# Performance work log

Measured on AMD Instinct MI355X. Metric: run time of the kernel, lower is better.

The kernel has to match this reference:

```python
import jax, jax.numpy as jnp
import numpy as np

B, N, K, F = 1, 50000, 16, 128
EPS = 1e-5

def _bn(h, gamma, beta):
    # BatchNorm1d in training mode: per-feature-channel stats over (batch, nodes)
    mean = jnp.mean(h, axis=(0, 1), keepdims=True)
    var = jnp.var(h, axis=(0, 1), keepdims=True)
    return (h - mean) * jax.lax.rsqrt(var + EPS) * gamma + beta

def _rgcn(h, neighbors, W, b):
    # pad one zero node row, gather K neighbors per node, flatten, linear
    h_pad = jnp.pad(h, ((0, 0), (0, 1), (0, 0)))           # [B, N+1, F]
    gathered = h_pad[:, neighbors]                          # [B, N, K, F]
    flat = gathered.reshape(h.shape[0], neighbors.shape[0], -1)  # [B, N, K*F]
    return jnp.einsum('bnk,ok->bno', flat, W) + b

def setup_inputs():
    key = jax.random.key(0)
    ks = jax.random.split(key, 10)
    x = jax.random.normal(ks[0], (B, N, F), jnp.float32)
    graph = jax.random.randint(ks[1], (N, K, 2), 0, N)
    gamma1 = 1.0 + 0.1 * jax.random.normal(ks[2], (F,), jnp.float32)
    beta1 = 0.1 * jax.random.normal(ks[3], (F,), jnp.float32)
    gamma2 = 1.0 + 0.1 * jax.random.normal(ks[4], (F,), jnp.float32)
    beta2 = 0.1 * jax.random.normal(ks[5], (F,), jnp.float32)
    s = 1.0 / np.sqrt(K * F)
    W1 = jax.random.uniform(ks[6], (F, K * F), jnp.float32, -s, s)
    b1 = jax.random.uniform(ks[7], (F,), jnp.float32, -s, s)
    W2 = jax.random.uniform(ks[8], (F, K * F), jnp.float32, -s, s)
    b2 = jax.random.uniform(ks[9], (F,), jnp.float32, -s, s)
    return {"x": x, "graph": graph, "gamma1": gamma1, "beta1": beta1,
            "W1": W1, "b1": b1, "gamma2": gamma2, "beta2": beta2,
            "W2": W2, "b2": b2}

def reference(x, graph, gamma1, beta1, W1, b1, gamma2, beta2, W2, b2):
    neighbors = graph[..., 1]                               # [N, K]
    out = jax.nn.gelu(_bn(x, gamma1, beta1), approximate=False)
    out = _rgcn(out, neighbors, W1, b1)                     # [B, N, F]
    out = jax.nn.gelu(_bn(out, gamma2, beta2), approximate=False)
    out = _rgcn(out, neighbors, W2, b2)                     # [B, N, F]
    return out + x
```

## Files before the change

kernel.cpp:

```cpp
#include <hip/hip_runtime.h>


#define NN 50000
#define FF 128

typedef __bf16 v8bf __attribute__((ext_vector_type(8)));
typedef float  v4f  __attribute__((ext_vector_type(4)));

__device__ __forceinline__ unsigned short f2bf(float f) {
  unsigned int u = __builtin_bit_cast(unsigned int, f);
  u += 0x7FFFu + ((u >> 16) & 1u);
  return (unsigned short)(u >> 16);
}
__device__ __forceinline__ float bf2f(unsigned short s) {
  unsigned int u = ((unsigned int)s) << 16;
  return __builtin_bit_cast(float, u);
}
__device__ __forceinline__ float gelu_f(float y) {
  return 0.5f * y * (1.0f + erff(y * 0.70710678118654752f));
}

__global__ void wconv_kernel(const float* __restrict__ W1, const float* __restrict__ W2,
                             unsigned short* __restrict__ Wt1, unsigned short* __restrict__ Wt2) {
  int t = blockIdx.x * 256 + threadIdx.x;
  const float* W = (t >= 32768) ? W2 : W1;
  unsigned short* Wt = (t >= 32768) ? Wt2 : Wt1;
  int r = t & 32767;
  int frag = r >> 6, lane = r & 63;
  int k4 = frag >> 3, c = frag & 7;
  int o  = c * 16 + (lane & 15);
  int kd = k4 * 32 + (lane >> 4) * 8;
  const float* src = W + o * 2048 + kd;
  unsigned short* dst = Wt + r * 8;
#pragma unroll
  for (int j = 0; j < 8; ++j) dst[j] = f2bf(src[j]);
}

__global__ void bn_stats_kernel(const float* __restrict__ x, float* __restrict__ part) {
  float s0=0,s1=0,s2=0,s3=0,q0=0,q1=0,q2=0,q3=0;
  for (int cb = blockIdx.x; cb < (NN*FF/1024); cb += 256) {
    float4 v = reinterpret_cast<const float4*>(x)[cb * 256 + threadIdx.x];
    s0+=v.x; q0+=v.x*v.x; s1+=v.y; q1+=v.y*v.y;
    s2+=v.z; q2+=v.z*v.z; s3+=v.w; q3+=v.w*v.w;
  }
  __shared__ float ls[1024], lsq[1024];
  int fb = (threadIdx.x & 31) * 4;
  int sl = threadIdx.x >> 5;
  ls[sl*128+fb]   = s0; ls[sl*128+fb+1]  = s1; ls[sl*128+fb+2]  = s2; ls[sl*128+fb+3]  = s3;
  lsq[sl*128+fb]  = q0; lsq[sl*128+fb+1] = q1; lsq[sl*128+fb+2] = q2; lsq[sl*128+fb+3] = q3;
  __syncthreads();
  if (threadIdx.x < 128) {
    float S=0,Q=0;
#pragma unroll
    for (int s2i=0; s2i<8; ++s2i){ S += ls[s2i*128+threadIdx.x]; Q += lsq[s2i*128+threadIdx.x]; }
    part[blockIdx.x*256 + threadIdx.x]       = S;
    part[blockIdx.x*256 + 128 + threadIdx.x] = Q;
  }
}

__global__ __launch_bounds__(1024) void bn_reduce_kernel(
    const float* __restrict__ part, int nb,
    const float* __restrict__ gamma, const float* __restrict__ beta,
    float* __restrict__ scsh) {
  int f = threadIdx.x & 127;
  int g = threadIdx.x >> 7;
  float S = 0.f, Q = 0.f;
  for (int b = g; b < nb; b += 8) {
    S += part[b * 256 + f];
    Q += part[b * 256 + 128 + f];
  }
  __shared__ float ls[8][128], lq[8][128];
  ls[g][f] = S; lq[g][f] = Q;
  __syncthreads();
  if (threadIdx.x < 128) {
    float St = 0.f, Qt = 0.f;
#pragma unroll
    for (int i = 0; i < 8; ++i) { St += ls[i][f]; Qt += lq[i][f]; }
    float inv  = 1.0f / (float)NN;
    float mean = St * inv;
    float var  = fmaxf(Qt * inv - mean * mean, 0.0f);
    float sc   = gamma[f] * rsqrtf(var + 1e-5f);
    scsh[f]       = sc;
    scsh[128 + f] = beta[f] - mean * sc;
  }
}

__global__ void apply1_kernel(const float* __restrict__ x, const float* __restrict__ scsh,
                              unsigned short* __restrict__ h1) {
  int stride = gridDim.x * blockDim.x;
  for (int c = blockIdx.x * blockDim.x + threadIdx.x; c < NN*FF/4; c += stride) {
    float4 v = reinterpret_cast<const float4*>(x)[c];
    int f = (c * 4) & 127;
    ushort4 o;
    o.x = f2bf(gelu_f(v.x * scsh[f]   + scsh[128+f]));
    o.y = f2bf(gelu_f(v.y * scsh[f+1] + scsh[128+f+1]));
    o.z = f2bf(gelu_f(v.z * scsh[f+2] + scsh[128+f+2]));
    o.w = f2bf(gelu_f(v.w * scsh[f+3] + scsh[128+f+3]));
    reinterpret_cast<ushort4*>(h1)[c] = o;
  }
}

__global__ void apply2_kernel(const unsigned short* __restrict__ t1, const float* __restrict__ scsh,
                              unsigned short* __restrict__ h2) {
  int stride = gridDim.x * blockDim.x;
  for (int c = blockIdx.x * blockDim.x + threadIdx.x; c < NN*FF/4; c += stride) {
    ushort4 v = reinterpret_cast<const ushort4*>(t1)[c];
    int f = (c * 4) & 127;
    ushort4 o;
    o.x = f2bf(gelu_f(bf2f(v.x) * scsh[f]   + scsh[128+f]));
    o.y = f2bf(gelu_f(bf2f(v.y) * scsh[f+1] + scsh[128+f+1]));
    o.z = f2bf(gelu_f(bf2f(v.z) * scsh[f+2] + scsh[128+f+2]));
    o.w = f2bf(gelu_f(bf2f(v.w) * scsh[f+3] + scsh[128+f+3]));
    reinterpret_cast<ushort4*>(h2)[c] = o;
  }
}

template<bool STATS>
__global__ __launch_bounds__(256) void rgcn_kernel(
    const unsigned short* __restrict__ h,
    const unsigned short* __restrict__ Wt,
    const int* __restrict__ graph,
    const float* __restrict__ bias,
    const float* __restrict__ xres,
    float* __restrict__ outf,
    unsigned short* __restrict__ outb,
    float* __restrict__ part)
{
  const int tid  = threadIdx.x;
  const int wv   = tid >> 6;
  const int lane = tid & 63;
  const int l15  = lane & 15;
  const int lq   = lane >> 4;
  const int nodebase = blockIdx.x * 128 + wv * 32;

  v4f acc[2][8];
#pragma unroll
  for (int rf = 0; rf < 2; ++rf)
#pragma unroll
    for (int c = 0; c < 8; ++c) acc[rf][c] = (v4f){0.f, 0.f, 0.f, 0.f};

  const int an0 = min(nodebase + l15, NN - 1);
  const int an1 = min(nodebase + 16 + l15, NN - 1);

  int ni0 = graph[(an0 * 16 + 0) * 2 + 1];
  int ni1 = graph[(an1 * 16 + 0) * 2 + 1];

#pragma unroll 1
  for (int k = 0; k < 16; ++k) {
    int i0 = min(max(ni0, 0), NN - 1);
    int i1 = min(max(ni1, 0), NN - 1);
    if (k < 15) {
      ni0 = graph[(an0 * 16 + k + 1) * 2 + 1];
      ni1 = graph[(an1 * 16 + k + 1) * 2 + 1];
    }
    const unsigned short* r0 = h + i0 * 128 + lq * 8;
    const unsigned short* r1 = h + i1 * 128 + lq * 8;
    v8bf a0[4], a1[4];
#pragma unroll
    for (int w4 = 0; w4 < 4; ++w4) {
      a0[w4] = *reinterpret_cast<const v8bf*>(r0 + w4 * 32);
      a1[w4] = *reinterpret_cast<const v8bf*>(r1 + w4 * 32);
    }
    const unsigned short* wp = Wt + (k * 4) * 4096 + lane * 8;
#pragma unroll
    for (int w4 = 0; w4 < 4; ++w4) {
#pragma unroll
      for (int c = 0; c < 8; ++c) {
        v8bf b = *reinterpret_cast<const v8bf*>(wp + w4 * 4096 + c * 512);
        acc[0][c] = __builtin_amdgcn_mfma_f32_16x16x32_bf16(a0[w4], b, acc[0][c], 0, 0, 0);
        acc[1][c] = __builtin_amdgcn_mfma_f32_16x16x32_bf16(a1[w4], b, acc[1][c], 0, 0, 0);
      }
    }
  }

  if constexpr (STATS) {
    __shared__ float lds_s[4][128];
    __shared__ float lds_q[4][128];
#pragma unroll
    for (int c = 0; c < 8; ++c) {
      float s = 0.f, q = 0.f;
#pragma unroll
      for (int rf = 0; rf < 2; ++rf) {
#pragma unroll
        for (int j = 0; j < 4; ++j) {
          int node = nodebase + rf * 16 + lq * 4 + j;
          float v  = acc[rf][c][j];
          if (node < NN) {
            s += v; q += v * v;
            outb[node * 128 + c * 16 + l15] = f2bf(v);
          }
        }
      }
      s += __shfl_xor(s, 16, 64); s += __shfl_xor(s, 32, 64);
      q += __shfl_xor(q, 16, 64); q += __shfl_xor(q, 32, 64);
      if (lq == 0) { lds_s[wv][c * 16 + l15] = s; lds_q[wv][c * 16 + l15] = q; }
    }
    __syncthreads();
    if (tid < 128) {
      float S = lds_s[0][tid] + lds_s[1][tid] + lds_s[2][tid] + lds_s[3][tid];
      float Q = lds_q[0][tid] + lds_q[1][tid] + lds_q[2][tid] + lds_q[3][tid];
      part[blockIdx.x * 256 + tid]       = S;
      part[blockIdx.x * 256 + 128 + tid] = Q;
    }
  } else {
#pragma unroll
    for (int c = 0; c < 8; ++c) {
      float bv = bias[c * 16 + l15];
#pragma unroll
      for (int rf = 0; rf < 2; ++rf) {
#pragma unroll
        for (int j = 0; j < 4; ++j) {
          int node = nodebase + rf * 16 + lq * 4 + j;
          if (node < NN) {
            int idx = node * 128 + c * 16 + l15;
            outf[idx] = acc[rf][c][j] + bv + xres[idx];
          }
        }
      }
    }
  }
}

extern "C" void kernel_launch(void* const* d_in, const int* in_sizes, int n_in,
                              void* d_out, int out_size, void* d_ws, size_t ws_size,
                              hipStream_t stream) {
  const float* x      = (const float*)d_in[0];
  const int*   graph  = (const int*)d_in[1];
  const float* gamma1 = (const float*)d_in[2];
  const float* beta1  = (const float*)d_in[3];
  const float* W1     = (const float*)d_in[4];
  const float* gamma2 = (const float*)d_in[6];
  const float* beta2  = (const float*)d_in[7];
  const float* W2     = (const float*)d_in[8];
  const float* b2     = (const float*)d_in[9];
  float* out = (float*)d_out;

  char* ws = (char*)d_ws;
  unsigned short* h1  = (unsigned short*)(ws);
  unsigned short* t1  = (unsigned short*)(ws + 12800000);
  unsigned short* Wt1 = (unsigned short*)(ws + 25600000);
  unsigned short* Wt2 = (unsigned short*)(ws + 26124288);
  float* p1    = (float*)(ws + 26648576);
  float* p2    = (float*)(ws + 26910720);
  float* scsh1 = (float*)(ws + 27311104);
  float* scsh2 = (float*)(ws + 27312128);

  wconv_kernel<<<256, 256, 0, stream>>>(W1, W2, Wt1, Wt2);
  bn_stats_kernel<<<256, 256, 0, stream>>>(x, p1);
  bn_reduce_kernel<<<1, 1024, 0, stream>>>(p1, 256, gamma1, beta1, scsh1);
  apply1_kernel<<<2048, 256, 0, stream>>>(x, scsh1, h1);
  rgcn_kernel<true><<<391, 256, 0, stream>>>(h1, Wt1, graph, nullptr, nullptr, nullptr, t1, p2);
  bn_reduce_kernel<<<1, 1024, 0, stream>>>(p2, 391, gamma2, beta2, scsh2);
  apply2_kernel<<<2048, 256, 0, stream>>>(t1, scsh2, h1);
  rgcn_kernel<false><<<391, 256, 0, stream>>>(h1, Wt2, graph, b2, x, out, nullptr, nullptr);
}
```

Before: 245.9 us.

## Split RGCN neighbor loop across wave pairs with LDS reduction and prefetch

Each block now covers 64 nodes instead of 128. Two wave pairs each handle half of the 16 neighbors and combine their partial accumulators through shared memory. Neighbor indices are loaded up front as vector loads, and the next neighbor row is prefetched with a double-buffered register set. The grid doubles to 782 blocks with a 3-blocks-per-SM occupancy hint, which should expose more parallelism and hide gather latency. The cost is an LDS reduction plus barrier, extra register and LDS pressure, and twice the weight reads per node, since each block covers fewer nodes.

```diff
diff --git a/kernel.cpp b/kernel.cpp
--- a/kernel.cpp
+++ b/kernel.cpp
@@ -116,7 +116,7 @@
 }
 
 template<bool STATS>
-__global__ __launch_bounds__(256) void rgcn_kernel(
+__global__ __launch_bounds__(256, 3) void rgcn_kernel(
     const unsigned short* __restrict__ h,
     const unsigned short* __restrict__ Wt,
     const int* __restrict__ graph,
@@ -131,7 +131,11 @@
   const int lane = tid & 63;
   const int l15  = lane & 15;
   const int lq   = lane >> 4;
-  const int nodebase = blockIdx.x * 128 + wv * 32;
+  const int ng   = wv & 1;
+  const int kh   = wv >> 1;
+  const int nodebase = blockIdx.x * 64 + ng * 32;
+
+  __shared__ float red[2][64][68];
 
   v4f acc[2][8];
 #pragma unroll
@@ -142,78 +146,116 @@
   const int an0 = min(nodebase + l15, NN - 1);
   const int an1 = min(nodebase + 16 + l15, NN - 1);
 
-  int ni0 = graph[(an0 * 16 + 0) * 2 + 1];
-  int ni1 = graph[(an1 * 16 + 0) * 2 + 1];
-
-#pragma unroll 1
-  for (int k = 0; k < 16; ++k) {
-    int i0 = min(max(ni0, 0), NN - 1);
-    int i1 = min(max(ni1, 0), NN - 1);
-    if (k < 15) {
-      ni0 = graph[(an0 * 16 + k + 1) * 2 + 1];
-      ni1 = graph[(an1 * 16 + k + 1) * 2 + 1];
-    }
-    const unsigned short* r0 = h + i0 * 128 + lq * 8;
-    const unsigned short* r1 = h + i1 * 128 + lq * 8;
-    v8bf a0[4], a1[4];
+  int idx0[8], idx1[8];
+  {
+    const int4* g0 = reinterpret_cast<const int4*>(graph + an0 * 32 + kh * 16);
+    const int4* g1 = reinterpret_cast<const int4*>(graph + an1 * 32 + kh * 16);
+    int4 t0[4], t1v[4];
+#pragma unroll
+    for (int j = 0; j < 4; ++j) { t0[j] = g0[j]; t1v[j] = g1[j]; }
+#pragma unroll
+    for (int j = 0; j < 4; ++j) {
+      idx0[2*j] = t0[j].y;  idx0[2*j+1] = t0[j].w;
+      idx1[2*j] = t1v[j].y; idx1[2*j+1] = t1v[j].w;
+    }
+  }
+
+  const unsigned short* wbase = Wt + (kh * 8) * 16384 + lane * 8;
+
+  v8bf a0[2][4], a1[2][4];
+  {
+    const unsigned short* r0 = h + idx0[0] * 128 + lq * 8;
+    const unsigned short* r1 = h + idx1[0] * 128 + lq * 8;
 #pragma unroll
     for (int w4 = 0; w4 < 4; ++w4) {
-      a0[w4] = *reinterpret_cast<const v8bf*>(r0 + w4 * 32);
-      a1[w4] = *reinterpret_cast<const v8bf*>(r1 + w4 * 32);
-    }
-    const unsigned short* wp = Wt + (k * 4) * 4096 + lane * 8;
+      a0[0][w4] = *reinterpret_cast<const v8bf*>(r0 + w4 * 32);
+      a1[0][w4] = *reinterpret_cast<const v8bf*>(r1 + w4 * 32);
+    }
+  }
+
+#pragma unroll
+  for (int s = 0; s < 8; ++s) {
+    const int cur = s & 1, nxt = cur ^ 1;
+    if (s < 7) {
+      const unsigned short* r0 = h + idx0[s+1] * 128 + lq * 8;
+      const unsigned short* r1 = h + idx1[s+1] * 128 + lq * 8;
+#pragma unroll
+      for (int w4 = 0; w4 < 4; ++w4) {
+        a0[nxt][w4] = *reinterpret_cast<const v8bf*>(r0 + w4 * 32);
+        a1[nxt][w4] = *reinterpret_cast<const v8bf*>(r1 + w4 * 32);
+      }
+    }
+    const unsigned short* wp = wbase + s * 16384;
 #pragma unroll
     for (int w4 = 0; w4 < 4; ++w4) {
 #pragma unroll
       for (int c = 0; c < 8; ++c) {
         v8bf b = *reinterpret_cast<const v8bf*>(wp + w4 * 4096 + c * 512);
-        acc[0][c] = __builtin_amdgcn_mfma_f32_16x16x32_bf16(a0[w4], b, acc[0][c], 0, 0, 0);
-        acc[1][c] = __builtin_amdgcn_mfma_f32_16x16x32_bf16(a1[w4], b, acc[1][c], 0, 0, 0);
-      }
-    }
+        acc[0][c] = __builtin_amdgcn_mfma_f32_16x16x32_bf16(a0[cur][w4], b, acc[0][c], 0, 0, 0);
+        acc[1][c] = __builtin_amdgcn_mfma_f32_16x16x32_bf16(a1[cur][w4], b, acc[1][c], 0, 0, 0);
+      }
+    }
+  }
+
+  if (kh == 1) {
+#pragma unroll
+    for (int rf = 0; rf < 2; ++rf)
+#pragma unroll
+      for (int c = 0; c < 8; ++c)
+        *reinterpret_cast<v4f*>(&red[ng][lane][(rf*8+c)*4]) = acc[rf][c];
+  }
+  __syncthreads();
+  if (kh == 0) {
+#pragma unroll
+    for (int rf = 0; rf < 2; ++rf)
+#pragma unroll
+      for (int c = 0; c < 8; ++c)
+        acc[rf][c] += *reinterpret_cast<const v4f*>(&red[ng][lane][(rf*8+c)*4]);
   }
 
   if constexpr (STATS) {
-    __shared__ float lds_s[4][128];
-    __shared__ float lds_q[4][128];
-#pragma unroll
-    for (int c = 0; c < 8; ++c) {
-      float s = 0.f, q = 0.f;
-#pragma unroll
-      for (int rf = 0; rf < 2; ++rf) {
-#pragma unroll
-        for (int j = 0; j < 4; ++j) {
-          int node = nodebase + rf * 16 + lq * 4 + j;
-          float v  = acc[rf][c][j];
-          if (node < NN) {
-            s += v; q += v * v;
-            outb[node * 128 + c * 16 + l15] = f2bf(v);
+    __shared__ float lds_s[2][128];
+    __shared__ float lds_q[2][128];
+    if (kh == 0) {
+#pragma unroll
+      for (int c = 0; c < 8; ++c) {
+        float s = 0.f, q = 0.f;
+#pragma unroll
+        for (int rf = 0; rf < 2; ++rf) {
+#pragma unroll
+          for (int j = 0; j < 4; ++j) {
+            int node = nodebase + rf * 16 + lq * 4 + j;
+            float v  = acc[rf][c][j];
+            if (node < NN) {
+              s += v; q += v * v;
+              outb[node * 128 + c * 16 + l15] = f2bf(v);
+            }
           }
         }
-      }
-      s += __shfl_xor(s, 16, 64); s += __shfl_xor(s, 32, 64);
-      q += __shfl_xor(q, 16, 64); q += __shfl_xor(q, 32, 64);
-      if (lq == 0) { lds_s[wv][c * 16 + l15] = s; lds_q[wv][c * 16 + l15] = q; }
+        s += __shfl_xor(s, 16, 64); s += __shfl_xor(s, 32, 64);
+        q += __shfl_xor(q, 16, 64); q += __shfl_xor(q, 32, 64);
+        if (lq == 0) { lds_s[ng][c * 16 + l15] = s; lds_q[ng][c * 16 + l15] = q; }
+      }
     }
     __syncthreads();
     if (tid < 128) {
-      float S = lds_s[0][tid] + lds_s[1][tid] + lds_s[2][tid] + lds_s[3][tid];
-      float Q = lds_q[0][tid] + lds_q[1][tid] + lds_q[2][tid] + lds_q[3][tid];
-      part[blockIdx.x * 256 + tid]       = S;
-      part[blockIdx.x * 256 + 128 + tid] = Q;
+      part[blockIdx.x * 256 + tid]       = lds_s[0][tid] + lds_s[1][tid];
+      part[blockIdx.x * 256 + 128 + tid] = lds_q[0][tid] + lds_q[1][tid];
     }
   } else {
-#pragma unroll
-    for (int c = 0; c < 8; ++c) {
-      float bv = bias[c * 16 + l15];
-#pragma unroll
-      for (int rf = 0; rf < 2; ++rf) {
-#pragma unroll
-        for (int j = 0; j < 4; ++j) {
-          int node = nodebase + rf * 16 + lq * 4 + j;
-          if (node < NN) {
-            int idx = node * 128 + c * 16 + l15;
-            outf[idx] = acc[rf][c][j] + bv + xres[idx];
+    if (kh == 0) {
+#pragma unroll
+      for (int c = 0; c < 8; ++c) {
+        float bv = bias[c * 16 + l15];
+#pragma unroll
+        for (int rf = 0; rf < 2; ++rf) {
+#pragma unroll
+          for (int j = 0; j < 4; ++j) {
+            int node = nodebase + rf * 16 + lq * 4 + j;
+            if (node < NN) {
+              int idx = node * 128 + c * 16 + l15;
+              outf[idx] = acc[rf][c][j] + bv + xres[idx];
+            }
           }
         }
       }
@@ -241,16 +283,16 @@
   unsigned short* Wt1 = (unsigned short*)(ws + 25600000);
   unsigned short* Wt2 = (unsigned short*)(ws + 26124288);
   float* p1    = (float*)(ws + 26648576);
-  float* p2    = (float*)(ws + 26910720);
-  float* scsh1 = (float*)(ws + 27311104);
-  float* scsh2 = (float*)(ws + 27312128);
+  float* p2    = p1;
+  float* scsh1 = (float*)(ws + 27449344);
+  float* scsh2 = (float*)(ws + 27450368);
 
   wconv_kernel<<<256, 256, 0, stream>>>(W1, W2, Wt1, Wt2);
   bn_stats_kernel<<<256, 256, 0, stream>>>(x, p1);
   bn_reduce_kernel<<<1, 1024, 0, stream>>>(p1, 256, gamma1, beta1, scsh1);
   apply1_kernel<<<2048, 256, 0, stream>>>(x, scsh1, h1);
-  rgcn_kernel<true><<<391, 256, 0, stream>>>(h1, Wt1, graph, nullptr, nullptr, nullptr, t1, p2);
-  bn_reduce_kernel<<<1, 1024, 0, stream>>>(p2, 391, gamma2, beta2, scsh2);
+  rgcn_kernel<true><<<782, 256, 0, stream>>>(h1, Wt1, graph, nullptr, nullptr, nullptr, t1, p2);
+  bn_reduce_kernel<<<1, 1024, 0, stream>>>(p2, 782, gamma2, beta2, scsh2);
   apply2_kernel<<<2048, 256, 0, stream>>>(t1, scsh2, h1);
-  rgcn_kernel<false><<<391, 256, 0, stream>>>(h1, Wt2, graph, b2, x, out, nullptr, nullptr);
-}
+  rgcn_kernel<false><<<782, 256, 0, stream>>>(h1, Wt2, graph, b2, x, out, nullptr, nullptr);
+}
```

After: 295.7 us. 20.2% more time.

## Use single-wave RGCN blocks with double-buffered neighbor gathers and preloaded indices

Applied to the files above, without the earlier changes.

The RGCN kernel now runs one wave per block over 32 nodes, launching 1563 blocks instead of 391 with 4 waves each. All 16 neighbor indices are loaded up front with vector int4 reads, and the next neighbor's feature rows are prefetched into a second register buffer while the current MFMAs run. This hides gather latency and removes the LDS reduction and the block barrier. Per-block partial stats are written to the output buffer as scratch. The costs are higher register pressure from the double buffer and full unroll, and four times more partials for bn_reduce to sum.

```diff
diff --git a/kernel.cpp b/kernel.cpp
--- a/kernel.cpp
+++ b/kernel.cpp
@@ -116,7 +116,7 @@
 }
 
 template<bool STATS>
-__global__ __launch_bounds__(256) void rgcn_kernel(
+__global__ __launch_bounds__(64) void rgcn_kernel(
     const unsigned short* __restrict__ h,
     const unsigned short* __restrict__ Wt,
     const int* __restrict__ graph,
@@ -126,12 +126,10 @@
     unsigned short* __restrict__ outb,
     float* __restrict__ part)
 {
-  const int tid  = threadIdx.x;
-  const int wv   = tid >> 6;
-  const int lane = tid & 63;
+  const int lane = threadIdx.x & 63;
   const int l15  = lane & 15;
   const int lq   = lane >> 4;
-  const int nodebase = blockIdx.x * 128 + wv * 32;
+  const int nodebase = blockIdx.x * 32;
 
   v4f acc[2][8];
 #pragma unroll
@@ -142,40 +140,52 @@
   const int an0 = min(nodebase + l15, NN - 1);
   const int an1 = min(nodebase + 16 + l15, NN - 1);
 
-  int ni0 = graph[(an0 * 16 + 0) * 2 + 1];
-  int ni1 = graph[(an1 * 16 + 0) * 2 + 1];
-
-#pragma unroll 1
-  for (int k = 0; k < 16; ++k) {
-    int i0 = min(max(ni0, 0), NN - 1);
-    int i1 = min(max(ni1, 0), NN - 1);
-    if (k < 15) {
-      ni0 = graph[(an0 * 16 + k + 1) * 2 + 1];
-      ni1 = graph[(an1 * 16 + k + 1) * 2 + 1];
-    }
-    const unsigned short* r0 = h + i0 * 128 + lq * 8;
-    const unsigned short* r1 = h + i1 * 128 + lq * 8;
-    v8bf a0[4], a1[4];
-#pragma unroll
-    for (int w4 = 0; w4 < 4; ++w4) {
-      a0[w4] = *reinterpret_cast<const v8bf*>(r0 + w4 * 32);
-      a1[w4] = *reinterpret_cast<const v8bf*>(r1 + w4 * 32);
-    }
-    const unsigned short* wp = Wt + (k * 4) * 4096 + lane * 8;
+  int idx0[16], idx1[16];
+  {
+    const int4* g0 = reinterpret_cast<const int4*>(graph + an0 * 32);
+    const int4* g1 = reinterpret_cast<const int4*>(graph + an1 * 32);
+#pragma unroll
+    for (int j = 0; j < 8; ++j) {
+      int4 t0 = g0[j], t1v = g1[j];
+      idx0[2*j]   = min(max(t0.y, 0), NN - 1);
+      idx0[2*j+1] = min(max(t0.w, 0), NN - 1);
+      idx1[2*j]   = min(max(t1v.y, 0), NN - 1);
+      idx1[2*j+1] = min(max(t1v.w, 0), NN - 1);
+    }
+  }
+
+  v8bf A0[2][4], A1[2][4];
+#define LOADA(buf, s_) {                                              \
+    const unsigned short* r0 = h + idx0[s_] * 128 + lq * 8;           \
+    const unsigned short* r1 = h + idx1[s_] * 128 + lq * 8;           \
+    _Pragma("unroll")                                                 \
+    for (int w4 = 0; w4 < 4; ++w4) {                                  \
+      A0[buf][w4] = *reinterpret_cast<const v8bf*>(r0 + w4 * 32);     \
+      A1[buf][w4] = *reinterpret_cast<const v8bf*>(r1 + w4 * 32);     \
+    }                                                                 \
+  }
+
+  LOADA(0, 0);
+  const unsigned short* wlane = Wt + lane * 8;
+
+#pragma unroll
+  for (int s = 0; s < 16; ++s) {
+    const int cur = s & 1;
+    if (s < 15) LOADA(cur ^ 1, s + 1);
+    const unsigned short* wp = wlane + s * 16384;
 #pragma unroll
     for (int w4 = 0; w4 < 4; ++w4) {
 #pragma unroll
       for (int c = 0; c < 8; ++c) {
         v8bf b = *reinterpret_cast<const v8bf*>(wp + w4 * 4096 + c * 512);
-        acc[0][c] = __builtin_amdgcn_mfma_f32_16x16x32_bf16(a0[w4], b, acc[0][c], 0, 0, 0);
-        acc[1][c] = __builtin_amdgcn_mfma_f32_16x16x32_bf16(a1[w4], b, acc[1][c], 0, 0, 0);
-      }
-    }
-  }
+        acc[0][c] = __builtin_amdgcn_mfma_f32_16x16x32_bf16(A0[cur][w4], b, acc[0][c], 0, 0, 0);
+        acc[1][c] = __builtin_amdgcn_mfma_f32_16x16x32_bf16(A1[cur][w4], b, acc[1][c], 0, 0, 0);
+      }
+    }
+  }
+#undef LOADA
 
   if constexpr (STATS) {
-    __shared__ float lds_s[4][128];
-    __shared__ float lds_q[4][128];
 #pragma unroll
     for (int c = 0; c < 8; ++c) {
       float s = 0.f, q = 0.f;
@@ -193,14 +203,10 @@
       }
       s += __shfl_xor(s, 16, 64); s += __shfl_xor(s, 32, 64);
       q += __shfl_xor(q, 16, 64); q += __shfl_xor(q, 32, 64);
-      if (lq == 0) { lds_s[wv][c * 16 + l15] = s; lds_q[wv][c * 16 + l15] = q; }
-    }
-    __syncthreads();
-    if (tid < 128) {
-      float S = lds_s[0][tid] + lds_s[1][tid] + lds_s[2][tid] + lds_s[3][tid];
-      float Q = lds_q[0][tid] + lds_q[1][tid] + lds_q[2][tid] + lds_q[3][tid];
-      part[blockIdx.x * 256 + tid]       = S;
-      part[blockIdx.x * 256 + 128 + tid] = Q;
+      if (lq == 0) {
+        part[blockIdx.x * 256 + c * 16 + l15]       = s;
+        part[blockIdx.x * 256 + 128 + c * 16 + l15] = q;
+      }
     }
   } else {
 #pragma unroll
@@ -241,16 +247,16 @@
   unsigned short* Wt1 = (unsigned short*)(ws + 25600000);
   unsigned short* Wt2 = (unsigned short*)(ws + 26124288);
   float* p1    = (float*)(ws + 26648576);
-  float* p2    = (float*)(ws + 26910720);
-  float* scsh1 = (float*)(ws + 27311104);
-  float* scsh2 = (float*)(ws + 27312128);
+  float* scsh1 = (float*)(ws + 26910720);
+  float* scsh2 = (float*)(ws + 26911744);
+  float* p2    = out;
 
   wconv_kernel<<<256, 256, 0, stream>>>(W1, W2, Wt1, Wt2);
   bn_stats_kernel<<<256, 256, 0, stream>>>(x, p1);
   bn_reduce_kernel<<<1, 1024, 0, stream>>>(p1, 256, gamma1, beta1, scsh1);
   apply1_kernel<<<2048, 256, 0, stream>>>(x, scsh1, h1);
-  rgcn_kernel<true><<<391, 256, 0, stream>>>(h1, Wt1, graph, nullptr, nullptr, nullptr, t1, p2);
-  bn_reduce_kernel<<<1, 1024, 0, stream>>>(p2, 391, gamma2, beta2, scsh2);
+  rgcn_kernel<true><<<1563, 64, 0, stream>>>(h1, Wt1, graph, nullptr, nullptr, nullptr, t1, p2);
+  bn_reduce_kernel<<<1, 1024, 0, stream>>>(p2, 1563, gamma2, beta2, scsh2);
   apply2_kernel<<<2048, 256, 0, stream>>>(t1, scsh2, h1);
-  rgcn_kernel<false><<<391, 256, 0, stream>>>(h1, Wt2, graph, b2, x, out, nullptr, nullptr);
-}
+  rgcn_kernel<false><<<1563, 64, 0, stream>>>(h1, Wt2, graph, b2, x, out, nullptr, nullptr);
+}
```

Result: slower. 397.9 us (+61.8%).

## Prefetch neighbor indices and software-pipeline gathers three steps ahead

Applied to the files above, without the earlier changes.

Each lane now loads all 16 neighbor indices up front with vectorized int4 reads instead of one scalar load per step. The K loop is fully unrolled, and the gathered neighbor rows are kept in a 4-deep register ring so the row loads for step k+3 are issued while MFMAs run on step k. The goal is to hide the latency of the random gathers behind matrix work. In exchange, register use rises sharply, and launch_bounds(256,1) is set to allow that, which may lower occupancy.

```diff
diff --git a/kernel.cpp b/kernel.cpp
--- a/kernel.cpp
+++ b/kernel.cpp
@@ -116,7 +116,7 @@
 }
 
 template<bool STATS>
-__global__ __launch_bounds__(256) void rgcn_kernel(
+__global__ __launch_bounds__(256, 1) void rgcn_kernel(
     const unsigned short* __restrict__ h,
     const unsigned short* __restrict__ Wt,
     const int* __restrict__ graph,
@@ -142,36 +142,57 @@
   const int an0 = min(nodebase + l15, NN - 1);
   const int an1 = min(nodebase + 16 + l15, NN - 1);
 
-  int ni0 = graph[(an0 * 16 + 0) * 2 + 1];
-  int ni1 = graph[(an1 * 16 + 0) * 2 + 1];
-
-#pragma unroll 1
-  for (int k = 0; k < 16; ++k) {
-    int i0 = min(max(ni0, 0), NN - 1);
-    int i1 = min(max(ni1, 0), NN - 1);
-    if (k < 15) {
-      ni0 = graph[(an0 * 16 + k + 1) * 2 + 1];
-      ni1 = graph[(an1 * 16 + k + 1) * 2 + 1];
-    }
-    const unsigned short* r0 = h + i0 * 128 + lq * 8;
-    const unsigned short* r1 = h + i1 * 128 + lq * 8;
-    v8bf a0[4], a1[4];
-#pragma unroll
-    for (int w4 = 0; w4 < 4; ++w4) {
-      a0[w4] = *reinterpret_cast<const v8bf*>(r0 + w4 * 32);
-      a1[w4] = *reinterpret_cast<const v8bf*>(r1 + w4 * 32);
-    }
-    const unsigned short* wp = Wt + (k * 4) * 4096 + lane * 8;
-#pragma unroll
-    for (int w4 = 0; w4 < 4; ++w4) {
-#pragma unroll
-      for (int c = 0; c < 8; ++c) {
-        v8bf b = *reinterpret_cast<const v8bf*>(wp + w4 * 4096 + c * 512);
-        acc[0][c] = __builtin_amdgcn_mfma_f32_16x16x32_bf16(a0[w4], b, acc[0][c], 0, 0, 0);
-        acc[1][c] = __builtin_amdgcn_mfma_f32_16x16x32_bf16(a1[w4], b, acc[1][c], 0, 0, 0);
-      }
-    }
-  }
+  int idx0[16], idx1[16];
+  {
+    const int4* g0 = reinterpret_cast<const int4*>(graph + an0 * 32);
+    const int4* g1 = reinterpret_cast<const int4*>(graph + an1 * 32);
+#pragma unroll
+    for (int j = 0; j < 8; ++j) {
+      int4 t0 = g0[j], t1v = g1[j];
+      idx0[2*j]   = min(max(t0.y,  0), NN - 1) * 128;
+      idx0[2*j+1] = min(max(t0.w,  0), NN - 1) * 128;
+      idx1[2*j]   = min(max(t1v.y, 0), NN - 1) * 128;
+      idx1[2*j+1] = min(max(t1v.w, 0), NN - 1) * 128;
+    }
+  }
+
+  v8bf A0[4][4], A1[4][4];
+#define GATHER(s_) {                                                  \
+    const unsigned short* r0 = h + idx0[s_] + lq * 8;                 \
+    const unsigned short* r1 = h + idx1[s_] + lq * 8;                 \
+    _Pragma("unroll")                                                 \
+    for (int w4 = 0; w4 < 4; ++w4) {                                  \
+      A0[(s_) & 3][w4] = *reinterpret_cast<const v8bf*>(r0 + w4*32);  \
+      A1[(s_) & 3][w4] = *reinterpret_cast<const v8bf*>(r1 + w4*32);  \
+    }                                                                 \
+  }
+
+  const unsigned short* wlane = Wt + lane * 8;
+
+  GATHER(0) GATHER(1) GATHER(2)
+
+#define BODY(t_) {                                                         \
+    const unsigned short* wp = wlane + (t_) * 16384;                       \
+    _Pragma("unroll")                                                      \
+    for (int w4 = 0; w4 < 4; ++w4) {                                       \
+      _Pragma("unroll")                                                    \
+      for (int c = 0; c < 8; ++c) {                                        \
+        v8bf b = *reinterpret_cast<const v8bf*>(wp + w4*4096 + c*512);     \
+        acc[0][c] = __builtin_amdgcn_mfma_f32_16x16x32_bf16(               \
+                      A0[(t_) & 3][w4], b, acc[0][c], 0, 0, 0);            \
+        acc[1][c] = __builtin_amdgcn_mfma_f32_16x16x32_bf16(               \
+                      A1[(t_) & 3][w4], b, acc[1][c], 0, 0, 0);            \
+      }                                                                    \
+    }                                                                      \
+    if ((t_) + 3 < 16) GATHER((t_) + 3)                                    \
+  }
+
+  BODY(0)  BODY(1)  BODY(2)  BODY(3)
+  BODY(4)  BODY(5)  BODY(6)  BODY(7)
+  BODY(8)  BODY(9)  BODY(10) BODY(11)
+  BODY(12) BODY(13) BODY(14) BODY(15)
+#undef BODY
+#undef GATHER
 
   if constexpr (STATS) {
     __shared__ float lds_s[4][128];
```

Result: slower. 340.4 us (+38.4%).
